# Kernel optimization log

Measured on AMD Instinct MI355X. Metric: run time of the kernel, lower is better.

The kernel has to match this reference:

```python
import jax, jax.numpy as jnp
import numpy as np

T, B, F = 512, 256, 1
H = 256          # hidden width of all GRU stacks
P = 256          # pred_classes
DELAY = 1
W_SCALE = 0.06   # ~1/sqrt(H), mimics torch GRUCell init scale


def setup_inputs() -> dict:
    key = jax.random.key(0)
    ks = jax.random.split(key, 24)
    rn = lambda k, shp, s=1.0: s * jax.random.normal(k, shp, dtype=jnp.float32)
    return {
        "sequence": rn(ks[0], (T, B, F)),
        "delay_pad": rn(ks[1], (DELAY, B, F)),
        "h0_enc": rn(ks[2], (B, H)),
        "h0_mask": rn(ks[3], (B, H)),
        "h0_pred": rn(ks[4], (B, H)),
        "enc_w_ih": rn(ks[5], (3 * H, F), W_SCALE),
        "enc_w_hh": rn(ks[6], (3 * H, H), W_SCALE),
        "enc_b_ih": rn(ks[7], (3 * H,), W_SCALE),
        "enc_b_hh": rn(ks[8], (3 * H,), W_SCALE),
        "mdec_w_ih": rn(ks[9], (3 * H, H), W_SCALE),
        "mdec_w_hh": rn(ks[10], (3 * H, H), W_SCALE),
        "mdec_b_ih": rn(ks[11], (3 * H,), W_SCALE),
        "mdec_b_hh": rn(ks[12], (3 * H,), W_SCALE),
        "mlin_w": rn(ks[13], (F, H), W_SCALE),
        "mlin_b": rn(ks[14], (F,), W_SCALE),
        "pdec_w_ih": rn(ks[15], (3 * H, H), W_SCALE),
        "pdec_w_hh": rn(ks[16], (3 * H, H), W_SCALE),
        "pdec_b_ih": rn(ks[17], (3 * H,), W_SCALE),
        "pdec_b_hh": rn(ks[18], (3 * H,), W_SCALE),
        "plin_w": rn(ks[19], (P, H), W_SCALE),
        "plin_b": rn(ks[20], (P,), W_SCALE),
    }


def gru_cell(x, h, w_ih, w_hh, b_ih, b_hh):
    # torch.nn.GRUCell semantics; gate order r, z, n in the stacked weights.
    gi = x @ w_ih.T + b_ih           # [B, 3H]
    gh = h @ w_hh.T + b_hh           # [B, 3H]
    i_r, i_z, i_n = jnp.split(gi, 3, axis=-1)
    h_r, h_z, h_n = jnp.split(gh, 3, axis=-1)
    r = jax.nn.sigmoid(i_r + h_r)
    z = jax.nn.sigmoid(i_z + h_z)
    n = jnp.tanh(i_n + r * h_n)
    return (1.0 - z) * n + z * h


def reference(sequence, delay_pad, h0_enc, h0_mask, h0_pred,
              enc_w_ih, enc_w_hh, enc_b_ih, enc_b_hh,
              mdec_w_ih, mdec_w_hh, mdec_b_ih, mdec_b_hh, mlin_w, mlin_b,
              pdec_w_ih, pdec_w_hh, pdec_b_ih, pdec_b_hh, plin_w, plin_b):
    # delay: prepend padding, drop last `delay` steps.  seq stays [T, B, F].
    seq = jnp.concatenate([delay_pad, sequence[:-DELAY]], axis=0)

    def step(carry, x_t):
        h_e, h_m, h_p = carry
        h_e = gru_cell(x_t, h_e, enc_w_ih, enc_w_hh, enc_b_ih, enc_b_hh)
        h_m = gru_cell(h_e, h_m, mdec_w_ih, mdec_w_hh, mdec_b_ih, mdec_b_hh)
        mask_t = h_m @ mlin_w.T + mlin_b      # [B, F]
        h_p = gru_cell(h_e, h_p, pdec_w_ih, pdec_w_hh, pdec_b_ih, pdec_b_hh)
        pred_t = h_p @ plin_w.T + plin_b      # [B, P]
        return (h_e, h_m, h_p), (mask_t, pred_t)

    _, (masks, preds) = jax.lax.scan(step, (h0_enc, h0_mask, h0_pred), seq)
    mask = masks.reshape(seq.shape)           # [T, B, F]
    pred = jnp.mean(preds, axis=0)            # [B, P]
    return mask, pred
```

## Files before the change

kernel.cpp:

```cpp
#include <hip/hip_runtime.h>
#include <hip/hip_fp16.h>

typedef _Float16 f16;
typedef _Float16 f16x8 __attribute__((ext_vector_type(8)));
typedef _Float16 f16x4 __attribute__((ext_vector_type(4)));
typedef float    f32x4 __attribute__((ext_vector_type(4)));
typedef unsigned long long u64;
typedef u64 u64x2 __attribute__((ext_vector_type(2)));

#define TT 512
#define BB 256
#define HH 256

#define O_WFRAG_ENC 0u
#define O_WFRAG_M   393216u
#define O_WFRAG_P   786432u
#define O_WFRAG_GI  1179648u
#define O_HE_ST     1966080u
#define O_HM_ST     2097152u
#define O_HP_ST     2228224u
#define O_HPSUM     2359296u
#define O_XCHG      2621440u
#define O_FLAGS     3407872u
#define O_DYN       3408896u
#define DYN_PER_STEP 917504u

__device__ __forceinline__ float sigf(float x){ return 1.0f/(1.0f+__expf(-x)); }
__device__ __forceinline__ float tanh_(float x){
  float xc = fminf(fmaxf(x,-15.f),15.f);
  float e  = __expf(2.f*xc);
  return (e-1.f)/(e+1.f);
}
__device__ __forceinline__ int hswz(int row, int j){
  return row*256 + ((((j>>3) ^ (row&7)))<<3) + (j&7);
}

__global__ void prep_kernel(
    const float* __restrict__ enc_whh, const float* __restrict__ mdec_whh,
    const float* __restrict__ pdec_whh, const float* __restrict__ mdec_wih,
    const float* __restrict__ pdec_wih,
    const float* __restrict__ h0e, const float* __restrict__ h0m, const float* __restrict__ h0p,
    f16* __restrict__ wfrag_enc, f16* __restrict__ wfrag_m, f16* __restrict__ wfrag_p,
    f16* __restrict__ wfrag_gi,
    f16* __restrict__ he_st, f16* __restrict__ hm_st, f16* __restrict__ hp_st,
    float* __restrict__ hpsum, int* __restrict__ flags)
{
  int idx = blockIdx.x*256 + threadIdx.x;
  const int NW = 16*3*8*64*8;
  if (idx < 3*NW){
    int b = idx / NW, e = idx % NW;
    int jj = e & 7, l = (e>>3)&63, ks = (e>>9)&7, t2 = e>>12;
    int g = t2 % 3, w = t2 / 3;
    int row = g*256 + w*16 + (l&15);
    int col = ks*32 + (l>>4)*8 + jj;
    const float* W = (b==0)?enc_whh:((b==1)?mdec_whh:pdec_whh);
    f16* D = (b==0)?wfrag_enc:((b==1)?wfrag_m:wfrag_p);
    D[e] = (f16)W[row*256+col];
    return;
  }
  idx -= 3*NW;
  const int NG = 96*8*64*8;
  if (idx < NG){
    int e = idx;
    int jj = e&7, l=(e>>3)&63, ks=(e>>9)&7, mt = e>>12;
    int row = mt*16 + (l&15);
    int col = ks*32 + (l>>4)*8 + jj;
    float v = (row < 768) ? mdec_wih[row*256+col] : pdec_wih[(row-768)*256+col];
    wfrag_gi[e] = (f16)v;
    return;
  }
  idx -= NG;
  if (idx < 65536){
    he_st[idx] = (f16)h0e[idx];
    hm_st[idx] = (f16)h0m[idx];
    hp_st[idx] = (f16)h0p[idx];
    hpsum[idx] = 0.f;
    if (idx < 96) flags[idx] = 0;
  }
}

template<int MODE>
__device__ __forceinline__ void gru_run(
  int role, int bt, int slice, int SL,
  const f16* __restrict__ wfrag,
  const float* __restrict__ bih, const float* __restrict__ bhh,
  const float* __restrict__ enc_wih,
  const float* __restrict__ seq, const float* __restrict__ dpad,
  const f16* __restrict__ gi_src,
  f16* __restrict__ h_state,
  f16* __restrict__ he_buf,
  const float* __restrict__ mlin_w, const float* __restrict__ mlin_b,
  float* __restrict__ out_mask,
  float* __restrict__ hpsum,
  u64* __restrict__ xchg, int* __restrict__ flags,
  unsigned char* smem)
{
  const int tid = threadIdx.x;
  const int lane = tid & 63;
  const int wid  = tid >> 6;
  const int l15  = lane & 15;
  const int lhi  = lane >> 4;
  const int bi0  = lhi*4;
  const int b0   = bt*16;
  constexpr int FREC = (MODE==1) ? 0 : ((MODE==2) ? 1 : 2);

  f16* hbuf   = (f16*)smem;
  float* xb   = (float*)(smem + 16384);
  float* mlwf = xb + 32;

  f16x8 wf[2][3][8];
  #pragma unroll
  for (int q=0;q<2;++q){
    const int w = role*8 + wid*2 + q;
    #pragma unroll
    for (int g=0;g<3;++g)
      #pragma unroll
      for (int ks=0;ks<8;++ks)
        wf[q][g][ks] = *(const f16x8*)(wfrag + ((size_t)(((w*3+g)*8)+ks)*64 + lane)*8);
  }
  #pragma unroll
  for (int q=0;q<2;++q)
    #pragma unroll
    for (int g=0;g<3;++g)
      #pragma unroll
      for (int ks=0;ks<8;++ks)
        asm volatile("" : "+v"(wf[q][g][ks]));

  float cr[2], cz[2], cnh[2], cni[2];
  float wr_[2], wz_[2], wn_[2];
  #pragma unroll
  for (int q=0;q<2;++q){
    const int j = (role*8 + wid*2 + q)*16 + l15;
    if (MODE==0){
      cr[q]  = bih[j]     + bhh[j];
      cz[q]  = bih[256+j] + bhh[256+j];
      cnh[q] = bhh[512+j];
      cni[q] = bih[512+j];
      wr_[q]=enc_wih[j]; wz_[q]=enc_wih[256+j]; wn_[q]=enc_wih[512+j];
    } else {
      cr[q]  = bhh[j];
      cz[q]  = bhh[256+j];
      cnh[q] = bhh[512+j];
    }
  }
  float mlb = 0.f;
  if (MODE==1 && role==0){
    mlwf[tid] = mlin_w[tid];
    mlb = mlin_b[0];
  }

  for (int jb=wid; jb<16; jb+=4){
    const int j = jb*16 + l15;
    #pragma unroll
    for (int r=0;r<4;++r)
      hbuf[hswz(bi0+r, j)] = h_state[(size_t)(b0+bi0+r)*256 + j];
  }
  if (MODE==0){
    if (tid<16){
      const int t = slice*SL;
      xb[tid] = (t==0) ? dpad[b0+tid] : seq[(size_t)(t-1)*BB + b0 + tid];
    }
  }
  __syncthreads();

  float psum[2][4];
  if (MODE==2){
    #pragma unroll
    for (int q=0;q<2;++q)
      #pragma unroll
      for (int r=0;r<4;++r) psum[q][r]=0.f;
  }

  const int fmy = (FREC*16 + bt)*2 + role;
  const int fpt = (FREC*16 + bt)*2 + (1-role);
  int* myf = flags + fmy;
  int* ptf = flags + fpt;

  for (int ts=0; ts<SL; ++ts){
    const int cur = ts & 1;
    f16* hc = hbuf + cur*4096;
    f16* hn = hbuf + (cur^1)*4096;
    const int gstep = slice*SL + ts;

    f16x4 gv[2][3];
    if (MODE!=0){
      const f16* gts = gi_src + (size_t)ts*393216u;
      #pragma unroll
      for (int q=0;q<2;++q)
        #pragma unroll
        for (int g=0;g<3;++g)
          gv[q][g] = *(const f16x4*)(gts + ((size_t)(g*256 + (role*8+wid*2+q)*16 + l15))*16 + bi0);
    } else {
      if (tid<16 && ts+1<SL)
        xb[(cur^1)*16 + tid] = seq[(size_t)(slice*SL + ts)*BB + b0 + tid];
    }

    if (MODE==1 && role==0 && ts>0){
      const int mb = tid>>4, jj = tid&15;
      float s = 0.f;
      #pragma unroll
      for (int k=0;k<16;++k){ const int j = jj + k*16; s += (float)hc[hswz(mb, j)]*mlwf[j]; }
      s += __shfl_xor(s,1,64); s += __shfl_xor(s,2,64);
      s += __shfl_xor(s,4,64); s += __shfl_xor(s,8,64);
      if (jj==0) out_mask[(size_t)(slice*SL + ts-1)*BB + b0 + mb] = s + mlb;
    }

    #pragma unroll
    for (int q=0;q<2;++q){
      const int j = (role*8 + wid*2 + q)*16 + l15;
      f32x4 a0 = {cr[q],cr[q],cr[q],cr[q]};
      f32x4 a1 = {cz[q],cz[q],cz[q],cz[q]};
      f32x4 a2 = {cnh[q],cnh[q],cnh[q],cnh[q]};
      #pragma unroll
      for (int ks=0;ks<8;++ks){
        const f16x8 a = *(const f16x8*)(hc + l15*256 + ((((ks*4+lhi) ^ (l15&7)))<<3));
        a0 = __builtin_amdgcn_mfma_f32_16x16x32_f16(a, wf[q][0][ks], a0, 0,0,0);
        a1 = __builtin_amdgcn_mfma_f32_16x16x32_f16(a, wf[q][1][ks], a1, 0,0,0);
        a2 = __builtin_amdgcn_mfma_f32_16x16x32_f16(a, wf[q][2][ks], a2, 0,0,0);
      }
      float gir[4], giz[4], gin[4];
      if (MODE==0){
        #pragma unroll
        for (int r=0;r<4;++r){
          const float x = xb[cur*16 + bi0 + r];
          gir[r]=x*wr_[q]; giz[r]=x*wz_[q]; gin[r]=x*wn_[q] + cni[q];
        }
      } else {
        #pragma unroll
        for (int r=0;r<4;++r){
          gir[r]=(float)gv[q][0][r]; giz[r]=(float)gv[q][1][r]; gin[r]=(float)gv[q][2][r];
        }
      }
      #pragma unroll
      for (int r=0;r<4;++r){
        const int sz = hswz(bi0+r, j);
        const float hprev = (float)hc[sz];
        const float rr = sigf(gir[r] + a0[r]);
        const float zz = sigf(giz[r] + a1[r]);
        const float nn = tanh_(gin[r] + rr*a2[r]);
        const float h  = (1.f-zz)*nn + zz*hprev;
        hn[sz] = (f16)h;
        if (MODE==0) he_buf[((size_t)ts*BB + (b0+bi0+r))*HH + j] = (f16)h;
        if (MODE==2) psum[q][r] += h;
      }
    }
    __syncthreads();

    {
      const int trow = tid>>4, tgl = tid&15;
      const int glo = tgl + role*16;
      const f16* sp = hn + trow*256 + ((glo ^ (trow&7))<<3);
      const u64x2 v = *(const u64x2*)sp;
      u64* dm = xchg + ((size_t)(fmy*2 + cur))*512 + tid*2;
      __hip_atomic_store(dm+0, v[0], __ATOMIC_RELAXED, __HIP_MEMORY_SCOPE_AGENT);
      __hip_atomic_store(dm+1, v[1], __ATOMIC_RELAXED, __HIP_MEMORY_SCOPE_AGENT);
    }
    __syncthreads();
    if (tid==0){
      __hip_atomic_store(myf, gstep+1, __ATOMIC_RELEASE, __HIP_MEMORY_SCOPE_AGENT);
      while (__hip_atomic_load(ptf, __ATOMIC_ACQUIRE, __HIP_MEMORY_SCOPE_AGENT) < gstep+1)
        __builtin_amdgcn_s_sleep(1);
    }
    __syncthreads();
    {
      const int trow = tid>>4, tgl = tid&15;
      const u64* dp = xchg + ((size_t)(fpt*2 + cur))*512 + tid*2;
      u64x2 v;
      v[0] = __hip_atomic_load(dp+0, __ATOMIC_RELAXED, __HIP_MEMORY_SCOPE_AGENT);
      v[1] = __hip_atomic_load(dp+1, __ATOMIC_RELAXED, __HIP_MEMORY_SCOPE_AGENT);
      const int glp = tgl + (1-role)*16;
      f16* dq = hn + trow*256 + ((glp ^ (trow&7))<<3);
      *(u64x2*)dq = v;
    }
    __syncthreads();
  }

  const f16* hf = hbuf + (SL&1)*4096;
  if (MODE==1 && role==0){
    const int mb = tid>>4, jj = tid&15;
    float s = 0.f;
    #pragma unroll
    for (int k=0;k<16;++k){ const int j = jj + k*16; s += (float)hf[hswz(mb, j)]*mlwf[j]; }
    s += __shfl_xor(s,1,64); s += __shfl_xor(s,2,64);
    s += __shfl_xor(s,4,64); s += __shfl_xor(s,8,64);
    if (jj==0) out_mask[(size_t)(slice*SL + SL-1)*BB + b0 + mb] = s + mlb;
  }
  #pragma unroll
  for (int q=0;q<2;++q){
    const int j = (role*8 + wid*2 + q)*16 + l15;
    #pragma unroll
    for (int r=0;r<4;++r)
      h_state[(size_t)(b0+bi0+r)*256 + j] = hf[hswz(bi0+r, j)];
  }
  if (MODE==2){
    #pragma unroll
    for (int q=0;q<2;++q){
      const int j = (role*8 + wid*2 + q)*16 + l15;
      #pragma unroll
      for (int r=0;r<4;++r){
        const size_t idx = (size_t)(b0+bi0+r)*256 + j;
        hpsum[idx] = hpsum[idx] + psum[q][r];
      }
    }
  }
}

__global__ __launch_bounds__(256,1) void rec_kernel(
  const float* __restrict__ seq, const float* __restrict__ dpad,
  const float* __restrict__ enc_wih, const float* __restrict__ enc_bih, const float* __restrict__ enc_bhh,
  const float* __restrict__ mdec_bhh, const float* __restrict__ pdec_bhh,
  const float* __restrict__ mlin_w, const float* __restrict__ mlin_b,
  const f16* __restrict__ wfrag_enc, const f16* __restrict__ wfrag_m, const f16* __restrict__ wfrag_p,
  f16* __restrict__ he_st, f16* __restrict__ hm_st, f16* __restrict__ hp_st,
  f16* __restrict__ he_buf, const f16* __restrict__ gi_buf,
  float* __restrict__ hpsum, float* __restrict__ out_mask,
  u64* __restrict__ xchg, int* __restrict__ flags,
  int dec_slice, int enc_slice, int SL)
{
  __shared__ __align__(16) unsigned char smem[16384 + 128 + 1024 + 512];
  const int bid = blockIdx.x;
  const int pp = bid % 48, role = bid / 48;
  if (pp < 16){
    if (dec_slice < 0) return;
    const int bt = pp;
    gru_run<1>(role, bt, dec_slice, SL, wfrag_m, nullptr, mdec_bhh, nullptr, nullptr, nullptr,
               gi_buf + (size_t)bt*1536*16, hm_st, nullptr, mlin_w, mlin_b, out_mask, nullptr,
               xchg, flags, smem);
  } else if (pp < 32){
    if (dec_slice < 0) return;
    const int bt = pp - 16;
    gru_run<2>(role, bt, dec_slice, SL, wfrag_p, nullptr, pdec_bhh, nullptr, nullptr, nullptr,
               gi_buf + ((size_t)bt*1536 + 768)*16, hp_st, nullptr, nullptr, nullptr, nullptr, hpsum,
               xchg, flags, smem);
  } else {
    if (enc_slice < 0) return;
    const int bt = pp - 32;
    gru_run<0>(role, bt, enc_slice, SL, wfrag_enc, enc_bih, enc_bhh, enc_wih, seq, dpad,
               nullptr, he_st, he_buf, nullptr, nullptr, nullptr, nullptr,
               xchg, flags, smem);
  }
}

__global__ __launch_bounds__(256,4) void gi_kernel(
  const f16* __restrict__ he_buf, const f16* __restrict__ wfrag_gi,
  const float* __restrict__ mdec_bih, const float* __restrict__ pdec_bih,
  f16* __restrict__ gi_buf)
{
  const int ts = blockIdx.x >> 2;
  const int bq = blockIdx.x & 3;
  const int tid = threadIdx.x, lane = tid&63, wid = tid>>6;
  const int l15 = lane&15, lhi = lane>>4;
  __shared__ f16 het[64*264];
  {
    const uint4* src = (const uint4*)(he_buf + ((size_t)ts*BB + bq*64)*HH);
    uint4* dst = (uint4*)het;
    #pragma unroll
    for (int k=0;k<8;++k){
      const int i = tid + k*256;
      dst[(i>>5)*33 + (i&31)] = src[i];
    }
  }
  __syncthreads();
  for (int mi=0; mi<24; ++mi){
    const int mt = wid*24 + mi;
    const int row0 = mt*16 + lhi*4;
    float bb[4];
    #pragma unroll
    for (int r=0;r<4;++r){
      const int rw = row0 + r;
      bb[r] = (rw < 768) ? mdec_bih[rw] : pdec_bih[rw-768];
    }
    f32x4 acc[4] = {{0,0,0,0},{0,0,0,0},{0,0,0,0},{0,0,0,0}};
    #pragma unroll
    for (int ks=0;ks<8;++ks){
      const f16x8 a = *(const f16x8*)(wfrag_gi + ((size_t)(mt*8+ks)*64 + lane)*8);
      #pragma unroll
      for (int bt=0;bt<4;++bt){
        const f16x8 b = *(const f16x8*)(het + (bt*16+l15)*264 + ks*32 + lhi*8);
        acc[bt] = __builtin_amdgcn_mfma_f32_16x16x32_f16(a, b, acc[bt], 0,0,0);
      }
    }
    #pragma unroll
    for (int bt=0;bt<4;++bt){
      const int btg = bq*4 + bt;
      const size_t base = (((size_t)ts*16 + btg)*1536 + (size_t)mt*16 + lhi*4)*16 + l15;
      #pragma unroll
      for (int r=0;r<4;++r) gi_buf[base + (size_t)r*16] = (f16)(acc[bt][r] + bb[r]);
    }
  }
}

__global__ __launch_bounds__(256,1) void pred_kernel(
  const float* __restrict__ hpsum, const float* __restrict__ plin_w,
  const float* __restrict__ plin_b, float* __restrict__ out)
{
  __shared__ float hs[256];
  const int p = threadIdx.x;
  const float bias = plin_b[p];
  for (int bb=0; bb<4; ++bb){
    const int b = blockIdx.x*4 + bb;
    __syncthreads();
    hs[p] = hpsum[(size_t)b*256 + p];
    __syncthreads();
    float acc = 0.f;
    const float4* wrow = (const float4*)(plin_w + (size_t)p*256);
    #pragma unroll 4
    for (int k4=0;k4<64;++k4){
      const float4 w = wrow[k4];
      acc += hs[k4*4+0]*w.x + hs[k4*4+1]*w.y + hs[k4*4+2]*w.z + hs[k4*4+3]*w.w;
    }
    out[131072 + (size_t)b*256 + p] = acc*(1.f/512.f) + bias;
  }
}

extern "C" void kernel_launch(void* const* d_in, const int* in_sizes, int n_in,
                              void* d_out, int out_size, void* d_ws, size_t ws_size,
                              hipStream_t stream)
{
  const float* seq      = (const float*)d_in[0];
  const float* dpad     = (const float*)d_in[1];
  const float* h0e      = (const float*)d_in[2];
  const float* h0m      = (const float*)d_in[3];
  const float* h0p      = (const float*)d_in[4];
  const float* enc_wih  = (const float*)d_in[5];
  const float* enc_whh  = (const float*)d_in[6];
  const float* enc_bih  = (const float*)d_in[7];
  const float* enc_bhh  = (const float*)d_in[8];
  const float* mdec_wih = (const float*)d_in[9];
  const float* mdec_whh = (const float*)d_in[10];
  const float* mdec_bih = (const float*)d_in[11];
  const float* mdec_bhh = (const float*)d_in[12];
  const float* mlin_w   = (const float*)d_in[13];
  const float* mlin_b   = (const float*)d_in[14];
  const float* pdec_wih = (const float*)d_in[15];
  const float* pdec_whh = (const float*)d_in[16];
  const float* pdec_bih = (const float*)d_in[17];
  const float* pdec_bhh = (const float*)d_in[18];
  const float* plin_w   = (const float*)d_in[19];
  const float* plin_b   = (const float*)d_in[20];
  float* out = (float*)d_out;

  char* ws = (char*)d_ws;
  f16* wfrag_enc = (f16*)(ws + O_WFRAG_ENC);
  f16* wfrag_m   = (f16*)(ws + O_WFRAG_M);
  f16* wfrag_p   = (f16*)(ws + O_WFRAG_P);
  f16* wfrag_gi  = (f16*)(ws + O_WFRAG_GI);
  f16* he_st     = (f16*)(ws + O_HE_ST);
  f16* hm_st     = (f16*)(ws + O_HM_ST);
  f16* hp_st     = (f16*)(ws + O_HP_ST);
  float* hpsum   = (float*)(ws + O_HPSUM);
  u64* xchg      = (u64*)(ws + O_XCHG);
  int* flags     = (int*)(ws + O_FLAGS);

  int SL = 64;
  while (SL > 1 && (size_t)O_DYN + (size_t)SL*DYN_PER_STEP > ws_size) SL >>= 1;
  const int S = TT / SL;
  f16* he_buf = (f16*)(ws + O_DYN);
  f16* gi_buf = (f16*)(ws + O_DYN + (size_t)SL*131072u);

  prep_kernel<<<dim3(4096), dim3(256), 0, stream>>>(
      enc_whh, mdec_whh, pdec_whh, mdec_wih, pdec_wih, h0e, h0m, h0p,
      wfrag_enc, wfrag_m, wfrag_p, wfrag_gi, he_st, hm_st, hp_st, hpsum, flags);

  rec_kernel<<<dim3(96), dim3(256), 0, stream>>>(
      seq, dpad, enc_wih, enc_bih, enc_bhh, mdec_bhh, pdec_bhh,
      mlin_w, mlin_b, wfrag_enc, wfrag_m, wfrag_p, he_st, hm_st, hp_st,
      he_buf, gi_buf, hpsum, out, xchg, flags, -1, 0, SL);
  gi_kernel<<<dim3(SL*4), dim3(256), 0, stream>>>(he_buf, wfrag_gi, mdec_bih, pdec_bih, gi_buf);

  for (int s=0; s<S; ++s){
    const int enc_s = (s+1 < S) ? (s+1) : -1;
    rec_kernel<<<dim3(96), dim3(256), 0, stream>>>(
        seq, dpad, enc_wih, enc_bih, enc_bhh, mdec_bhh, pdec_bhh,
        mlin_w, mlin_b, wfrag_enc, wfrag_m, wfrag_p, he_st, hm_st, hp_st,
        he_buf, gi_buf, hpsum, out, xchg, flags, s, enc_s, SL);
    if (enc_s >= 0)
      gi_kernel<<<dim3(SL*4), dim3(256), 0, stream>>>(he_buf, wfrag_gi, mdec_bih, pdec_bih, gi_buf);
  }

  pred_kernel<<<dim3(64), dim3(256), 0, stream>>>(hpsum, plin_w, plin_b, out);
}
```

Measured before the change: 3.918 ms.

## Split each GRU batch tile across four blocks with LDS-resident weights

Each recurrent batch tile is now handled by four cooperating blocks instead of two, so the kernel launches 192 blocks rather than 96. Each block owns a quarter of the hidden units. Recurrent weight fragments move from registers into 96KB of LDS, loaded with global_load_lds. Hidden-state exchange now goes through a four-way flag and xchg protocol, so each block waits on three peers per step. The aim is to halve per-block matmul work on the serial critical path, at the cost of more cross-block synchronization and LDS weight reads every step.

```diff
diff --git a/kernel.cpp b/kernel.cpp
--- a/kernel.cpp
+++ b/kernel.cpp
@@ -6,7 +6,6 @@
 typedef _Float16 f16x4 __attribute__((ext_vector_type(4)));
 typedef float    f32x4 __attribute__((ext_vector_type(4)));
 typedef unsigned long long u64;
-typedef u64 u64x2 __attribute__((ext_vector_type(2)));
 
 #define TT 512
 #define BB 256
@@ -34,6 +33,11 @@
 __device__ __forceinline__ int hswz(int row, int j){
   return row*256 + ((((j>>3) ^ (row&7)))<<3) + (j&7);
 }
+__device__ __forceinline__ void gload_lds16(const void* g, void* l){
+  __builtin_amdgcn_global_load_lds(
+      (const __attribute__((address_space(1))) unsigned int*)g,
+      (__attribute__((address_space(3))) unsigned int*)l, 16, 0, 0);
+}
 
 __global__ void prep_kernel(
     const float* __restrict__ enc_whh, const float* __restrict__ mdec_whh,
@@ -75,13 +79,13 @@
     hm_st[idx] = (f16)h0m[idx];
     hp_st[idx] = (f16)h0p[idx];
     hpsum[idx] = 0.f;
-    if (idx < 96) flags[idx] = 0;
+    if (idx < 192) flags[idx] = 0;
   }
 }
 
 template<int MODE>
 __device__ __forceinline__ void gru_run(
-  int role, int bt, int slice, int SL,
+  int q, int bt, int slice, int SL,
   const f16* __restrict__ wfrag,
   const float* __restrict__ bih, const float* __restrict__ bhh,
   const float* __restrict__ enc_wih,
@@ -103,78 +107,56 @@
   const int bi0  = lhi*4;
   const int b0   = bt*16;
   constexpr int FREC = (MODE==1) ? 0 : ((MODE==2) ? 1 : 2);
-
-  f16* hbuf   = (f16*)smem;
-  float* xb   = (float*)(smem + 16384);
+  const int jb = q*4 + wid;
+  const int j  = jb*16 + l15;
+
+  f16* wlds = (f16*)smem;
+  f16* hbuf = (f16*)(smem + 98304);
+  float* xb   = (float*)(smem + 98304 + 16384);
   float* mlwf = xb + 32;
 
-  f16x8 wf[2][3][8];
-  #pragma unroll
-  for (int q=0;q<2;++q){
-    const int w = role*8 + wid*2 + q;
-    #pragma unroll
-    for (int g=0;g<3;++g)
-      #pragma unroll
-      for (int ks=0;ks<8;++ks)
-        wf[q][g][ks] = *(const f16x8*)(wfrag + ((size_t)(((w*3+g)*8)+ks)*64 + lane)*8);
-  }
-  #pragma unroll
-  for (int q=0;q<2;++q)
-    #pragma unroll
-    for (int g=0;g<3;++g)
-      #pragma unroll
-      for (int ks=0;ks<8;++ks)
-        asm volatile("" : "+v"(wf[q][g][ks]));
-
-  float cr[2], cz[2], cnh[2], cni[2];
-  float wr_[2], wz_[2], wn_[2];
-  #pragma unroll
-  for (int q=0;q<2;++q){
-    const int j = (role*8 + wid*2 + q)*16 + l15;
-    if (MODE==0){
-      cr[q]  = bih[j]     + bhh[j];
-      cz[q]  = bih[256+j] + bhh[256+j];
-      cnh[q] = bhh[512+j];
-      cni[q] = bih[512+j];
-      wr_[q]=enc_wih[j]; wz_[q]=enc_wih[256+j]; wn_[q]=enc_wih[512+j];
-    } else {
-      cr[q]  = bhh[j];
-      cz[q]  = bhh[256+j];
-      cnh[q] = bhh[512+j];
-    }
+  {
+    const char* src = (const char*)wfrag + (size_t)q*98304u;
+    #pragma unroll
+    for (int c=0;c<24;++c){
+      gload_lds16(src + c*4096 + wid*1024 + (lane<<4),
+                  (char*)wlds + c*4096 + wid*1024);
+    }
+  }
+
+  float cr, cz, cnh, cni=0.f, wr_=0.f, wz_=0.f, wn_=0.f;
+  if (MODE==0){
+    cr  = bih[j]     + bhh[j];
+    cz  = bih[256+j] + bhh[256+j];
+    cnh = bhh[512+j];
+    cni = bih[512+j];
+    wr_ = enc_wih[j]; wz_ = enc_wih[256+j]; wn_ = enc_wih[512+j];
+  } else {
+    cr = bhh[j]; cz = bhh[256+j]; cnh = bhh[512+j];
   }
   float mlb = 0.f;
-  if (MODE==1 && role==0){
-    mlwf[tid] = mlin_w[tid];
-    mlb = mlin_b[0];
-  }
-
-  for (int jb=wid; jb<16; jb+=4){
-    const int j = jb*16 + l15;
+  if (MODE==1 && q==0){ mlwf[tid] = mlin_w[tid]; mlb = mlin_b[0]; }
+
+  for (int jb2=wid; jb2<16; jb2+=4){
+    const int j2 = jb2*16 + l15;
     #pragma unroll
     for (int r=0;r<4;++r)
-      hbuf[hswz(bi0+r, j)] = h_state[(size_t)(b0+bi0+r)*256 + j];
-  }
-  if (MODE==0){
-    if (tid<16){
-      const int t = slice*SL;
-      xb[tid] = (t==0) ? dpad[b0+tid] : seq[(size_t)(t-1)*BB + b0 + tid];
-    }
+      hbuf[hswz(bi0+r, j2)] = h_state[(size_t)(b0+bi0+r)*256 + j2];
+  }
+  if (MODE==0 && tid<16){
+    const int t = slice*SL;
+    xb[tid] = (t==0) ? dpad[b0+tid] : seq[(size_t)(t-1)*BB + b0 + tid];
   }
   __syncthreads();
 
-  float psum[2][4];
+  float psum[4];
   if (MODE==2){
     #pragma unroll
-    for (int q=0;q<2;++q)
-      #pragma unroll
-      for (int r=0;r<4;++r) psum[q][r]=0.f;
-  }
-
-  const int fmy = (FREC*16 + bt)*2 + role;
-  const int fpt = (FREC*16 + bt)*2 + (1-role);
-  int* myf = flags + fmy;
-  int* ptf = flags + fpt;
+    for (int r=0;r<4;++r) psum[r]=0.f;
+  }
+
+  const int gbase = (FREC*16 + bt)*4;
+  int* myf = flags + gbase + q;
 
   for (int ts=0; ts<SL; ++ts){
     const int cur = ts & 1;
@@ -182,53 +164,52 @@
     f16* hn = hbuf + (cur^1)*4096;
     const int gstep = slice*SL + ts;
 
-    f16x4 gv[2][3];
+    f16x4 gv0, gv1, gv2;
     if (MODE!=0){
       const f16* gts = gi_src + (size_t)ts*393216u;
-      #pragma unroll
-      for (int q=0;q<2;++q)
-        #pragma unroll
-        for (int g=0;g<3;++g)
-          gv[q][g] = *(const f16x4*)(gts + ((size_t)(g*256 + (role*8+wid*2+q)*16 + l15))*16 + bi0);
-    } else {
-      if (tid<16 && ts+1<SL)
-        xb[(cur^1)*16 + tid] = seq[(size_t)(slice*SL + ts)*BB + b0 + tid];
-    }
-
-    if (MODE==1 && role==0 && ts>0){
+      gv0 = *(const f16x4*)(gts + ((size_t)(      j))*16 + bi0);
+      gv1 = *(const f16x4*)(gts + ((size_t)(256 + j))*16 + bi0);
+      gv2 = *(const f16x4*)(gts + ((size_t)(512 + j))*16 + bi0);
+    } else if (tid<16 && ts+1<SL){
+      xb[(cur^1)*16 + tid] = seq[(size_t)(slice*SL + ts)*BB + b0 + tid];
+    }
+
+    if (MODE==1 && q==0 && ts>0){
       const int mb = tid>>4, jj = tid&15;
       float s = 0.f;
       #pragma unroll
-      for (int k=0;k<16;++k){ const int j = jj + k*16; s += (float)hc[hswz(mb, j)]*mlwf[j]; }
+      for (int k=0;k<16;++k){ const int jm = jj + k*16; s += (float)hc[hswz(mb, jm)]*mlwf[jm]; }
       s += __shfl_xor(s,1,64); s += __shfl_xor(s,2,64);
       s += __shfl_xor(s,4,64); s += __shfl_xor(s,8,64);
       if (jj==0) out_mask[(size_t)(slice*SL + ts-1)*BB + b0 + mb] = s + mlb;
     }
 
-    #pragma unroll
-    for (int q=0;q<2;++q){
-      const int j = (role*8 + wid*2 + q)*16 + l15;
-      f32x4 a0 = {cr[q],cr[q],cr[q],cr[q]};
-      f32x4 a1 = {cz[q],cz[q],cz[q],cz[q]};
-      f32x4 a2 = {cnh[q],cnh[q],cnh[q],cnh[q]};
-      #pragma unroll
-      for (int ks=0;ks<8;++ks){
-        const f16x8 a = *(const f16x8*)(hc + l15*256 + ((((ks*4+lhi) ^ (l15&7)))<<3));
-        a0 = __builtin_amdgcn_mfma_f32_16x16x32_f16(a, wf[q][0][ks], a0, 0,0,0);
-        a1 = __builtin_amdgcn_mfma_f32_16x16x32_f16(a, wf[q][1][ks], a1, 0,0,0);
-        a2 = __builtin_amdgcn_mfma_f32_16x16x32_f16(a, wf[q][2][ks], a2, 0,0,0);
-      }
+    f32x4 a0 = {cr,cr,cr,cr};
+    f32x4 a1 = {cz,cz,cz,cz};
+    f32x4 a2 = {cnh,cnh,cnh,cnh};
+    #pragma unroll
+    for (int ks=0;ks<8;++ks){
+      const f16x8 a  = *(const f16x8*)(hc + l15*256 + ((((ks*4+lhi) ^ (l15&7)))<<3));
+      const f16x8 b0f = *(const f16x8*)(wlds + ((size_t)(((wid*3+0)*8)+ks)*64 + lane)*8);
+      const f16x8 b1f = *(const f16x8*)(wlds + ((size_t)(((wid*3+1)*8)+ks)*64 + lane)*8);
+      const f16x8 b2f = *(const f16x8*)(wlds + ((size_t)(((wid*3+2)*8)+ks)*64 + lane)*8);
+      a0 = __builtin_amdgcn_mfma_f32_16x16x32_f16(a, b0f, a0, 0,0,0);
+      a1 = __builtin_amdgcn_mfma_f32_16x16x32_f16(a, b1f, a1, 0,0,0);
+      a2 = __builtin_amdgcn_mfma_f32_16x16x32_f16(a, b2f, a2, 0,0,0);
+    }
+
+    {
       float gir[4], giz[4], gin[4];
       if (MODE==0){
         #pragma unroll
         for (int r=0;r<4;++r){
           const float x = xb[cur*16 + bi0 + r];
-          gir[r]=x*wr_[q]; giz[r]=x*wz_[q]; gin[r]=x*wn_[q] + cni[q];
+          gir[r]=x*wr_; giz[r]=x*wz_; gin[r]=x*wn_ + cni;
         }
       } else {
         #pragma unroll
         for (int r=0;r<4;++r){
-          gir[r]=(float)gv[q][0][r]; giz[r]=(float)gv[q][1][r]; gin[r]=(float)gv[q][2][r];
+          gir[r]=(float)gv0[r]; giz[r]=(float)gv1[r]; gin[r]=(float)gv2[r];
         }
       }
       #pragma unroll
@@ -241,66 +222,59 @@
         const float h  = (1.f-zz)*nn + zz*hprev;
         hn[sz] = (f16)h;
         if (MODE==0) he_buf[((size_t)ts*BB + (b0+bi0+r))*HH + j] = (f16)h;
-        if (MODE==2) psum[q][r] += h;
+        if (MODE==2) psum[r] += h;
       }
     }
     __syncthreads();
 
     {
-      const int trow = tid>>4, tgl = tid&15;
-      const int glo = tgl + role*16;
-      const f16* sp = hn + trow*256 + ((glo ^ (trow&7))<<3);
-      const u64x2 v = *(const u64x2*)sp;
-      u64* dm = xchg + ((size_t)(fmy*2 + cur))*512 + tid*2;
-      __hip_atomic_store(dm+0, v[0], __ATOMIC_RELAXED, __HIP_MEMORY_SCOPE_AGENT);
-      __hip_atomic_store(dm+1, v[1], __ATOMIC_RELAXED, __HIP_MEMORY_SCOPE_AGENT);
-    }
-    __syncthreads();
-    if (tid==0){
+      const int row = tid>>4, o8 = tid&15;
+      const u64 v = *(const u64*)((const char*)hn + row*512 + q*128 + o8*8);
+      __hip_atomic_store(xchg + ((size_t)((gbase+q)*2 + cur))*256 + tid, v,
+                         __ATOMIC_RELAXED, __HIP_MEMORY_SCOPE_AGENT);
+    }
+    __syncthreads();
+    if (tid==0)
       __hip_atomic_store(myf, gstep+1, __ATOMIC_RELEASE, __HIP_MEMORY_SCOPE_AGENT);
+    if (tid<3){
+      const int pk = tid + (tid>=q ? 1 : 0);
+      int* ptf = flags + gbase + pk;
       while (__hip_atomic_load(ptf, __ATOMIC_ACQUIRE, __HIP_MEMORY_SCOPE_AGENT) < gstep+1)
         __builtin_amdgcn_s_sleep(1);
     }
     __syncthreads();
     {
-      const int trow = tid>>4, tgl = tid&15;
-      const u64* dp = xchg + ((size_t)(fpt*2 + cur))*512 + tid*2;
-      u64x2 v;
-      v[0] = __hip_atomic_load(dp+0, __ATOMIC_RELAXED, __HIP_MEMORY_SCOPE_AGENT);
-      v[1] = __hip_atomic_load(dp+1, __ATOMIC_RELAXED, __HIP_MEMORY_SCOPE_AGENT);
-      const int glp = tgl + (1-role)*16;
-      f16* dq = hn + trow*256 + ((glp ^ (trow&7))<<3);
-      *(u64x2*)dq = v;
+      const int row = tid>>4, o8 = tid&15;
+      #pragma unroll
+      for (int pi=0; pi<3; ++pi){
+        const int pk = pi + (pi>=q ? 1 : 0);
+        const u64 v = __hip_atomic_load(
+            xchg + ((size_t)((gbase+pk)*2 + cur))*256 + tid,
+            __ATOMIC_RELAXED, __HIP_MEMORY_SCOPE_AGENT);
+        *(u64*)((char*)hn + row*512 + pk*128 + o8*8) = v;
+      }
     }
     __syncthreads();
   }
 
   const f16* hf = hbuf + (SL&1)*4096;
-  if (MODE==1 && role==0){
+  if (MODE==1 && q==0){
     const int mb = tid>>4, jj = tid&15;
     float s = 0.f;
     #pragma unroll
-    for (int k=0;k<16;++k){ const int j = jj + k*16; s += (float)hf[hswz(mb, j)]*mlwf[j]; }
+    for (int k=0;k<16;++k){ const int jm = jj + k*16; s += (float)hf[hswz(mb, jm)]*mlwf[jm]; }
     s += __shfl_xor(s,1,64); s += __shfl_xor(s,2,64);
     s += __shfl_xor(s,4,64); s += __shfl_xor(s,8,64);
     if (jj==0) out_mask[(size_t)(slice*SL + SL-1)*BB + b0 + mb] = s + mlb;
   }
   #pragma unroll
-  for (int q=0;q<2;++q){
-    const int j = (role*8 + wid*2 + q)*16 + l15;
-    #pragma unroll
-    for (int r=0;r<4;++r)
-      h_state[(size_t)(b0+bi0+r)*256 + j] = hf[hswz(bi0+r, j)];
-  }
+  for (int r=0;r<4;++r)
+    h_state[(size_t)(b0+bi0+r)*256 + j] = hf[hswz(bi0+r, j)];
   if (MODE==2){
     #pragma unroll
-    for (int q=0;q<2;++q){
-      const int j = (role*8 + wid*2 + q)*16 + l15;
-      #pragma unroll
-      for (int r=0;r<4;++r){
-        const size_t idx = (size_t)(b0+bi0+r)*256 + j;
-        hpsum[idx] = hpsum[idx] + psum[q][r];
-      }
+    for (int r=0;r<4;++r){
+      const size_t idx = (size_t)(b0+bi0+r)*256 + j;
+      hpsum[idx] = hpsum[idx] + psum[r];
     }
   }
 }
@@ -317,25 +291,25 @@
   u64* __restrict__ xchg, int* __restrict__ flags,
   int dec_slice, int enc_slice, int SL)
 {
-  __shared__ __align__(16) unsigned char smem[16384 + 128 + 1024 + 512];
+  __shared__ __align__(16) unsigned char smem[98304 + 16384 + 128 + 1024 + 512];
   const int bid = blockIdx.x;
-  const int pp = bid % 48, role = bid / 48;
+  const int q = bid & 3, pp = bid >> 2;
   if (pp < 16){
     if (dec_slice < 0) return;
     const int bt = pp;
-    gru_run<1>(role, bt, dec_slice, SL, wfrag_m, nullptr, mdec_bhh, nullptr, nullptr, nullptr,
+    gru_run<1>(q, bt, dec_slice, SL, wfrag_m, nullptr, mdec_bhh, nullptr, nullptr, nullptr,
                gi_buf + (size_t)bt*1536*16, hm_st, nullptr, mlin_w, mlin_b, out_mask, nullptr,
                xchg, flags, smem);
   } else if (pp < 32){
     if (dec_slice < 0) return;
     const int bt = pp - 16;
-    gru_run<2>(role, bt, dec_slice, SL, wfrag_p, nullptr, pdec_bhh, nullptr, nullptr, nullptr,
+    gru_run<2>(q, bt, dec_slice, SL, wfrag_p, nullptr, pdec_bhh, nullptr, nullptr, nullptr,
                gi_buf + ((size_t)bt*1536 + 768)*16, hp_st, nullptr, nullptr, nullptr, nullptr, hpsum,
                xchg, flags, smem);
   } else {
     if (enc_slice < 0) return;
     const int bt = pp - 32;
-    gru_run<0>(role, bt, enc_slice, SL, wfrag_enc, enc_bih, enc_bhh, enc_wih, seq, dpad,
+    gru_run<0>(q, bt, enc_slice, SL, wfrag_enc, enc_bih, enc_bhh, enc_wih, seq, dpad,
                nullptr, he_st, he_buf, nullptr, nullptr, nullptr, nullptr,
                xchg, flags, smem);
   }
@@ -462,7 +436,7 @@
       enc_whh, mdec_whh, pdec_whh, mdec_wih, pdec_wih, h0e, h0m, h0p,
       wfrag_enc, wfrag_m, wfrag_p, wfrag_gi, he_st, hm_st, hp_st, hpsum, flags);
 
-  rec_kernel<<<dim3(96), dim3(256), 0, stream>>>(
+  rec_kernel<<<dim3(192), dim3(256), 0, stream>>>(
       seq, dpad, enc_wih, enc_bih, enc_bhh, mdec_bhh, pdec_bhh,
       mlin_w, mlin_b, wfrag_enc, wfrag_m, wfrag_p, he_st, hm_st, hp_st,
       he_buf, gi_buf, hpsum, out, xchg, flags, -1, 0, SL);
@@ -470,7 +444,7 @@
 
   for (int s=0; s<S; ++s){
     const int enc_s = (s+1 < S) ? (s+1) : -1;
-    rec_kernel<<<dim3(96), dim3(256), 0, stream>>>(
+    rec_kernel<<<dim3(192), dim3(256), 0, stream>>>(
         seq, dpad, enc_wih, enc_bih, enc_bhh, mdec_bhh, pdec_bhh,
         mlin_w, mlin_b, wfrag_enc, wfrag_m, wfrag_p, he_st, hm_st, hp_st,
         he_buf, gi_buf, hpsum, out, xchg, flags, s, enc_s, SL);
```

New measurement: 4.227 ms. 7.9% more time.
